# Kernel tuning notes

Hardware: AMD Instinct MI355X
Metric: run time of the kernel (lower is better)

Reference implementation:

```python
import jax, jax.numpy as jnp
import numpy as np

L = 2        # num_layers
D = 512      # d_model
H = 8        # heads
C = 512      # GAT per-head out channels (= d_model, concat=False -> mean over heads)
B, S, E = 4, 512, 4096
NEG = jnp.float32(-1e9)


def setup_inputs() -> dict:
    key = jax.random.key(0)
    ks = jax.random.split(key, 20)
    sc = 0.02  # weight init scale
    inp = {
        'x': jax.random.normal(ks[0], (B, S, D), jnp.float32),
        'Wq': jax.random.normal(ks[1], (L, D, D), jnp.float32) * sc,
        'bq': jnp.zeros((L, D), jnp.float32),
        'Wk': jax.random.normal(ks[2], (L, D, D), jnp.float32) * sc,
        'bk': jnp.zeros((L, D), jnp.float32),
        'Wv': jax.random.normal(ks[3], (L, D, D), jnp.float32) * sc,
        'bv': jnp.zeros((L, D), jnp.float32),
        'Wo': jax.random.normal(ks[4], (L, D, D), jnp.float32) * sc,
        'bo': jnp.zeros((L, D), jnp.float32),
        'gatW': jax.random.normal(ks[5], (L, D, H * C), jnp.float32) * sc,
        'att_src': jax.random.normal(ks[6], (L, H, C), jnp.float32) * sc,
        'att_dst': jax.random.normal(ks[7], (L, H, C), jnp.float32) * sc,
        'gat_bias': jnp.zeros((L, C), jnp.float32),
        'ln_g': jnp.ones((L, D), jnp.float32),
        'ln_b': jnp.zeros((L, D), jnp.float32),
        'input_len': jax.random.randint(ks[8], (B,), S // 2, S + 1, jnp.int32),
        'edges': jax.random.randint(ks[9], (B, 2, E), 0, S // 2, jnp.int32),
        'edge_num': jax.random.randint(ks[10], (B,), E // 2, E + 1, jnp.int32),
    }
    return inp


def layer_norm(x, g, b, eps=1e-5):
    m = x.mean(-1, keepdims=True)
    v = ((x - m) ** 2).mean(-1, keepdims=True)
    return (x - m) * jax.lax.rsqrt(v + eps) * g + b


def mha(x, pad_mask, Wq, bq, Wk, bk, Wv, bv, Wo, bo):
    # pad_mask: [B,S] True where padded (masked out)
    b, s, d = x.shape
    dh = d // H
    q = (x @ Wq + bq).reshape(b, s, H, dh)
    k = (x @ Wk + bk).reshape(b, s, H, dh)
    v = (x @ Wv + bv).reshape(b, s, H, dh)
    scores = jnp.einsum('bqhd,bkhd->bhqk', q, k) / jnp.float32(np.sqrt(dh))
    scores = jnp.where(pad_mask[:, None, None, :], NEG, scores)
    a = jax.nn.softmax(scores, axis=-1)
    o = jnp.einsum('bhqk,bkhd->bqhd', a, v).reshape(b, s, d)
    return o @ Wo + bo


def gat_single(x, edge_index, edge_mask, node_mask, W, a_src_w, a_dst_w, bias):
    # x: [S,D]; edge_index: [2,E]; GATConv(d_model,d_model,heads,concat=False)
    s = x.shape[0]
    h = (x @ W).reshape(s, H, C)
    a_src_n = (h * a_src_w).sum(-1)  # [S,H]
    a_dst_n = (h * a_dst_w).sum(-1)  # [S,H]
    # add self loops (PyG default) for valid nodes
    ar = jnp.arange(s, dtype=edge_index.dtype)
    src = jnp.concatenate([edge_index[0], ar])
    dst = jnp.concatenate([edge_index[1], ar])
    em = jnp.concatenate([edge_mask, node_mask])  # [E+S]
    alpha = jax.nn.leaky_relu(a_src_n[src] + a_dst_n[dst], 0.2)  # [E+S,H]
    alpha = jnp.where(em[:, None], alpha, NEG)
    amax = jax.ops.segment_max(alpha, dst, num_segments=s)  # [S,H]
    ex = jnp.exp(alpha - amax[dst]) * em[:, None].astype(alpha.dtype)
    denom = jax.ops.segment_sum(ex, dst, num_segments=s)
    coef = ex / (denom[dst] + 1e-16)
    msg = h[src] * coef[:, :, None]  # [E+S,H,C]
    out = jax.ops.segment_sum(msg, dst, num_segments=s)  # [S,H,C]
    return out.mean(axis=1) + bias  # concat=False -> mean over heads


def reference(x, Wq, bq, Wk, bk, Wv, bv, Wo, bo, gatW, att_src, att_dst,
              gat_bias, ln_g, ln_b, input_len, edges, edge_num):
    b, s, d = x.shape
    node_mask = jnp.arange(s)[None, :] < input_len[:, None]      # [B,S]
    edge_mask = jnp.arange(edges.shape[-1])[None, :] < edge_num[:, None]  # [B,E]
    pad_mask = ~node_mask
    out = x
    layer_outputs = []
    gat_b = jax.vmap(gat_single, in_axes=(0, 0, 0, 0, None, None, None, None))
    for i in range(L):
        out = mha(out, pad_mask, Wq[i], bq[i], Wk[i], bk[i], Wv[i], bv[i], Wo[i], bo[i])
        g = gat_b(out, edges, edge_mask, node_mask,
                  gatW[i], att_src[i], att_dst[i], gat_bias[i])
        y = jax.nn.relu(layer_norm(g, ln_g[i], ln_b[i])) + out
        out = jnp.where(node_mask[:, :, None], y, out)
        layer_outputs.append(out)
    return jnp.stack(layer_outputs)  # [L,B,S,D]
```

## Files before the change

### kernel.cpp

```cpp
#include <hip/hip_runtime.h>
#include <cstddef>

#define DMODEL 512
#define HEADS  8
#define DH     64
#define CCH    512
#define BATCH  4
#define SEQ    512
#define NEDGE  4096
#define NLAYER 2
#define HC     (HEADS*CCH)

typedef unsigned short bf16_t;
typedef __attribute__((ext_vector_type(8))) short short8;
typedef __attribute__((ext_vector_type(4))) float floatx4;

__device__ __forceinline__ bf16_t f2bf(float f){
  unsigned u = __float_as_uint(f);
  unsigned r = (u + 0x7FFFu + ((u>>16)&1u)) >> 16;
  return (bf16_t)r;
}
__device__ __forceinline__ float bf2f(bf16_t u){ return __uint_as_float(((unsigned)u)<<16); }

__global__ void k_zero(int* __restrict__ p, int n){
  int i = blockIdx.x*256 + threadIdx.x;
  if (i < n) p[i] = 0;
}

__global__ void k_f2b(const float* __restrict__ in, bf16_t* __restrict__ out, int n4){
  int i = blockIdx.x*256 + threadIdx.x;
  if (i < n4){
    float4 v = ((const float4*)in)[i];
    ushort4 o;
    o.x=f2bf(v.x); o.y=f2bf(v.y); o.z=f2bf(v.z); o.w=f2bf(v.w);
    ((ushort4*)out)[i]=o;
  }
}

__global__ __launch_bounds__(256) void k_wt(const float* __restrict__ W, bf16_t* __restrict__ WT,
                                            int K, int N){
  __shared__ float T[32][65];
  int n0 = blockIdx.x*64, k0 = blockIdx.y*32;
  int tid = threadIdx.x;
  int lk = tid>>3, ln = (tid&7)*8;
  const float* src = W + (size_t)(k0+lk)*N + n0 + ln;
  float4 v0 = *(const float4*)src;
  float4 v1 = *(const float4*)(src+4);
  T[lk][ln+0]=v0.x; T[lk][ln+1]=v0.y; T[lk][ln+2]=v0.z; T[lk][ln+3]=v0.w;
  T[lk][ln+4]=v1.x; T[lk][ln+5]=v1.y; T[lk][ln+6]=v1.z; T[lk][ln+7]=v1.w;
  __syncthreads();
  int wn = tid>>2, wk = (tid&3)*8;
  ushort4 o0, o1;
  o0.x=f2bf(T[wk+0][wn]); o0.y=f2bf(T[wk+1][wn]); o0.z=f2bf(T[wk+2][wn]); o0.w=f2bf(T[wk+3][wn]);
  o1.x=f2bf(T[wk+4][wn]); o1.y=f2bf(T[wk+5][wn]); o1.z=f2bf(T[wk+6][wn]); o1.w=f2bf(T[wk+7][wn]);
  bf16_t* dst = WT + (size_t)(n0+wn)*K + k0 + wk;
  *(ushort4*)dst = o0;
  *(ushort4*)(dst+4) = o1;
}

struct GemmB {
  const bf16_t* W; const float* bias; float* C; bf16_t* Cb;
  const float* att_s; const float* att_d; float* asrc; float* adst;
};
struct GemmB3 { GemmB g[3]; };

template<int BM, int BN>
__global__ __launch_bounds__(256) void k_gemm_mfma(const bf16_t* __restrict__ A, GemmB3 p,
                                                   int N, int K){
  constexpr int MI = BM/32;
  constexpr int NJ = BN/32;
  constexpr int ACH = BM/64;
  constexpr int BCH = BN/64;
  const GemmB& g = p.g[blockIdx.z];
  const bf16_t* Wt  = g.W;
  const float* bias = g.bias;
  float* C          = g.C;
  bf16_t* Cb        = g.Cb;
  __shared__ __align__(16) bf16_t As[BM*40];
  __shared__ __align__(16) bf16_t Bs[BN*40];
  int bm = blockIdx.x*BM, bn = blockIdx.y*BN;
  int tid = threadIdx.x;
  int wave = tid>>6, lane = tid&63;
  int wy = wave>>1, wx = wave&1;
  int quad = lane>>4, l16 = lane&15;
  floatx4 acc[MI][NJ];
  #pragma unroll
  for (int i=0;i<MI;i++)
    #pragma unroll
    for (int j=0;j<NJ;j++) acc[i][j] = (floatx4){0.f,0.f,0.f,0.f};
  int sr = tid>>2;
  int sc = (tid&3)<<3;
  for (int k0=0;k0<K;k0+=32){
    uint4 av[ACH], bv[BCH];
    #pragma unroll
    for (int c=0;c<ACH;c++) av[c] = *(const uint4*)(A  + (size_t)(bm+sr+c*64)*K + k0 + sc);
    #pragma unroll
    for (int c=0;c<BCH;c++) bv[c] = *(const uint4*)(Wt + (size_t)(bn+sr+c*64)*K + k0 + sc);
    __syncthreads();
    #pragma unroll
    for (int c=0;c<ACH;c++) *(uint4*)(As + (size_t)(sr+c*64)*40 + sc) = av[c];
    #pragma unroll
    for (int c=0;c<BCH;c++) *(uint4*)(Bs + (size_t)(sr+c*64)*40 + sc) = bv[c];
    __syncthreads();
    short8 af[MI], bfr[NJ];
    #pragma unroll
    for (int i=0;i<MI;i++) af[i]  = *(const short8*)(As + (size_t)(wy*(BM/2)+i*16+l16)*40 + quad*8);
    #pragma unroll
    for (int j=0;j<NJ;j++) bfr[j] = *(const short8*)(Bs + (size_t)(wx*(BN/2)+j*16+l16)*40 + quad*8);
    #pragma unroll
    for (int i=0;i<MI;i++)
      #pragma unroll
      for (int j=0;j<NJ;j++)
        acc[i][j] = __builtin_amdgcn_mfma_f32_16x16x32_bf16(af[i], bfr[j], acc[i][j], 0,0,0);
  }
  #pragma unroll
  for (int i=0;i<MI;i++){
    int row = bm + wy*(BM/2) + i*16 + quad*4;
    #pragma unroll
    for (int j=0;j<NJ;j++){
      int col = bn + wx*(BN/2) + j*16 + l16;
      float bi = bias ? bias[col] : 0.f;
      #pragma unroll
      for (int r=0;r<4;r++){
        float vvv = acc[i][j][r] + bi;
        if (C)  C[(size_t)(row+r)*N + col] = vvv;
        if (Cb) Cb[(size_t)(row+r)*N + col] = f2bf(vvv);
      }
    }
  }
  if (g.asrc){
    int colbase = bn + wx*(BN/2);
    int hidx = colbase >> 9;
    float aw_s[NJ], aw_d[NJ];
    #pragma unroll
    for (int j=0;j<NJ;j++){
      int col = colbase + j*16 + l16;
      aw_s[j] = g.att_s[col];
      aw_d[j] = g.att_d[col];
    }
    #pragma unroll
    for (int i=0;i<MI;i++){
      #pragma unroll
      for (int r=0;r<4;r++){
        float ps=0.f, pd=0.f;
        #pragma unroll
        for (int j=0;j<NJ;j++){ ps += acc[i][j][r]*aw_s[j]; pd += acc[i][j][r]*aw_d[j]; }
        #pragma unroll
        for (int m2=1;m2<16;m2<<=1){ ps += __shfl_xor(ps,m2); pd += __shfl_xor(pd,m2); }
        if (l16==0){
          int row = bm + wy*(BM/2) + i*16 + quad*4 + r;
          atomicAdd(&g.asrc[row*HEADS + hidx], ps);
          atomicAdd(&g.adst[row*HEADS + hidx], pd);
        }
      }
    }
  }
}

__global__ __launch_bounds__(256) void k_attn_flash(const bf16_t* __restrict__ q,
    const bf16_t* __restrict__ k, const bf16_t* __restrict__ v,
    const int* __restrict__ input_len, bf16_t* __restrict__ o){
  __shared__ __align__(16) bf16_t Kt[64*72];
  __shared__ __align__(16) bf16_t Vt[64*72];
  __shared__ __align__(16) bf16_t Pt[4][16*72];
  int q0 = blockIdx.x*64;
  int h  = blockIdx.y, b = blockIdx.z;
  int len = input_len[b];
  int tid = threadIdx.x;
  int w = tid>>6, lane = tid&63;
  int quad = lane>>4, l16 = lane&15;
  const bf16_t* qrow = q + ((size_t)(b*SEQ + q0 + w*16 + l16))*DMODEL + h*DH;
  short8 qa0 = *(const short8*)(qrow + quad*8);
  short8 qa1 = *(const short8*)(qrow + quad*8 + 32);
  int kr = tid>>2, kc = (tid&3)<<4;
  int vr = lane,   vc = w<<4;
  const bf16_t* kbase = k + ((size_t)(b*SEQ))*DMODEL + h*DH;
  const bf16_t* vbase = v + ((size_t)(b*SEQ))*DMODEL + h*DH;
  floatx4 oacc[4];
  #pragma unroll
  for (int dt=0;dt<4;dt++) oacc[dt] = (floatx4){0.f,0.f,0.f,0.f};
  float mrun[4], lrun[4];
  #pragma unroll
  for (int r=0;r<4;r++){ mrun[r]=-1e30f; lrun[r]=0.f; }
  for (int kt=0; kt<SEQ; kt+=64){
    if (kt >= len) break;
    uint4 kv0 = *(const uint4*)(kbase + (size_t)(kt+kr)*DMODEL + kc);
    uint4 kv1 = *(const uint4*)(kbase + (size_t)(kt+kr)*DMODEL + kc + 8);
    uint4 vv0 = *(const uint4*)(vbase + (size_t)(kt+vr)*DMODEL + vc);
    uint4 vv1 = *(const uint4*)(vbase + (size_t)(kt+vr)*DMODEL + vc + 8);
    __syncthreads();
    *(uint4*)(Kt + kr*72 + kc)     = kv0;
    *(uint4*)(Kt + kr*72 + kc + 8) = kv1;
    const ushort* vp0 = (const ushort*)&vv0;
    const ushort* vp1 = (const ushort*)&vv1;
    #pragma unroll
    for (int i2=0;i2<8;i2++) Vt[(vc+i2)*72 + vr]   = vp0[i2];
    #pragma unroll
    for (int i2=0;i2<8;i2++) Vt[(vc+8+i2)*72 + vr] = vp1[i2];
    __syncthreads();
    floatx4 sacc[4];
    #pragma unroll
    for (int nt=0;nt<4;nt++){
      sacc[nt] = (floatx4){0.f,0.f,0.f,0.f};
      short8 kb0 = *(const short8*)(Kt + (nt*16+l16)*72 + quad*8);
      short8 kb1 = *(const short8*)(Kt + (nt*16+l16)*72 + quad*8 + 32);
      sacc[nt] = __builtin_amdgcn_mfma_f32_16x16x32_bf16(qa0, kb0, sacc[nt], 0,0,0);
      sacc[nt] = __builtin_amdgcn_mfma_f32_16x16x32_bf16(qa1, kb1, sacc[nt], 0,0,0);
    }
    #pragma unroll
    for (int nt=0;nt<4;nt++){
      bool valid = (kt + nt*16 + l16) < len;
      #pragma unroll
      for (int r=0;r<4;r++){
        float sv = sacc[nt][r]*0.125f;
        sacc[nt][r] = valid ? sv : -1e30f;
      }
    }
    float alpha[4];
    #pragma unroll
    for (int r=0;r<4;r++){
      float mx = fmaxf(fmaxf(sacc[0][r],sacc[1][r]), fmaxf(sacc[2][r],sacc[3][r]));
      #pragma unroll
      for (int off=1; off<16; off<<=1) mx = fmaxf(mx, __shfl_xor(mx, off));
      float mn = fmaxf(mrun[r], mx);
      alpha[r] = __expf(mrun[r]-mn);
      mrun[r] = mn;
      float rs = 0.f;
      #pragma unroll
      for (int nt=0;nt<4;nt++){
        float pp = __expf(sacc[nt][r]-mn);
        sacc[nt][r] = pp; rs += pp;
      }
      #pragma unroll
      for (int off=1; off<16; off<<=1) rs += __shfl_xor(rs, off);
      lrun[r] = lrun[r]*alpha[r] + rs;
    }
    #pragma unroll
    for (int dt=0;dt<4;dt++)
      #pragma unroll
      for (int r=0;r<4;r++) oacc[dt][r] *= alpha[r];
    bf16_t* pw = Pt[w];
    #pragma unroll
    for (int nt=0;nt<4;nt++)
      #pragma unroll
      for (int r=0;r<4;r++) pw[(quad*4+r)*72 + nt*16 + l16] = f2bf(sacc[nt][r]);
    short8 pa0 = *(const short8*)(pw + l16*72 + quad*8);
    short8 pa1 = *(const short8*)(pw + l16*72 + quad*8 + 32);
    #pragma unroll
    for (int dt=0;dt<4;dt++){
      short8 vb0 = *(const short8*)(Vt + (dt*16+l16)*72 + quad*8);
      short8 vb1 = *(const short8*)(Vt + (dt*16+l16)*72 + quad*8 + 32);
      oacc[dt] = __builtin_amdgcn_mfma_f32_16x16x32_bf16(pa0, vb0, oacc[dt], 0,0,0);
      oacc[dt] = __builtin_amdgcn_mfma_f32_16x16x32_bf16(pa1, vb1, oacc[dt], 0,0,0);
    }
  }
  bf16_t* obase = o + ((size_t)(b*SEQ + q0 + w*16 + quad*4))*DMODEL + h*DH;
  #pragma unroll
  for (int r=0;r<4;r++){
    float invl = 1.f/lrun[r];
    #pragma unroll
    for (int dt=0;dt<4;dt++)
      obase[(size_t)r*DMODEL + dt*16 + l16] = f2bf(oacc[dt][r]*invl);
  }
}

__global__ void k_count(const int* __restrict__ edges, const int* __restrict__ edge_num, int* __restrict__ cnt){
  int b = blockIdx.y;
  int e = blockIdx.x*256 + threadIdx.x;
  if (e >= NEDGE || e >= edge_num[b]) return;
  int dst = edges[(size_t)b*2*NEDGE + NEDGE + e];
  atomicAdd(&cnt[b*SEQ + dst], 1);
}
__global__ void k_prefix(const int* __restrict__ cnt, int* __restrict__ offs, int* __restrict__ cursor){
  if (threadIdx.x==0){
    int b = blockIdx.x, acc=0;
    for (int s=0;s<SEQ;s++){ offs[b*SEQ+s]=acc; cursor[b*SEQ+s]=acc; acc+=cnt[b*SEQ+s]; }
  }
}
__global__ void k_fill(const int* __restrict__ edges, const int* __restrict__ edge_num,
                       int* __restrict__ cursor, int* __restrict__ elist){
  int b = blockIdx.y;
  int e = blockIdx.x*256 + threadIdx.x;
  if (e >= NEDGE || e >= edge_num[b]) return;
  int dst = edges[(size_t)b*2*NEDGE + NEDGE + e];
  int pos = atomicAdd(&cursor[b*SEQ + dst], 1);
  elist[(size_t)b*NEDGE + pos] = e;
}

__global__ __launch_bounds__(256) void k_gat_agg(const bf16_t* __restrict__ hbuf,
    const float* __restrict__ asrc, const float* __restrict__ adst,
    const int* __restrict__ offs, const int* __restrict__ cnt, const int* __restrict__ elist,
    const int* __restrict__ edges, const int* __restrict__ input_len,
    const float* __restrict__ gat_bias, float* __restrict__ gout){
  int s = blockIdx.x, b = blockIdx.y;
  if (s >= input_len[b]) return;
  __shared__ float amax_s[8], den_s[8], adl[8];
  __shared__ float cf[32][8];
  __shared__ int   cs[32];
  int tid = threadIdx.x;
  int n = cnt[b*SEQ+s];
  const int* el = elist + (size_t)b*NEDGE + offs[b*SEQ+s];
  const int* srcrow = edges + (size_t)b*2*NEDGE;
  if (tid < 8) adl[tid] = adst[(b*SEQ+s)*HEADS + tid];
  __syncthreads();
  if (tid < 64){
    float mx[8];
    #pragma unroll
    for (int h2=0;h2<8;h2++) mx[h2] = -1e30f;
    for (int j = tid; j <= n; j += 64){
      int src = (j==n) ? s : srcrow[el[j]];
      const float* ap = asrc + (size_t)(b*SEQ+src)*HEADS;
      #pragma unroll
      for (int h2=0;h2<8;h2++){
        float a = ap[h2] + adl[h2];
        a = (a>0.f)? a : 0.2f*a;
        mx[h2] = fmaxf(mx[h2], a);
      }
    }
    #pragma unroll
    for (int h2=0;h2<8;h2++){
      float vmx = mx[h2];
      #pragma unroll
      for (int off=32; off; off>>=1) vmx = fmaxf(vmx, __shfl_xor(vmx,off,64));
      mx[h2]=vmx;
    }
    float sm[8];
    #pragma unroll
    for (int h2=0;h2<8;h2++) sm[h2]=0.f;
    for (int j = tid; j <= n; j += 64){
      int src = (j==n) ? s : srcrow[el[j]];
      const float* ap = asrc + (size_t)(b*SEQ+src)*HEADS;
      #pragma unroll
      for (int h2=0;h2<8;h2++){
        float a = ap[h2] + adl[h2];
        a = (a>0.f)? a : 0.2f*a;
        sm[h2] += __expf(a - mx[h2]);
      }
    }
    #pragma unroll
    for (int h2=0;h2<8;h2++){
      float vs = sm[h2];
      #pragma unroll
      for (int off=32; off; off>>=1) vs += __shfl_xor(vs,off,64);
      if (tid==0){ amax_s[h2]=mx[h2]; den_s[h2]=vs; }
    }
  }
  __syncthreads();
  float acc0=0.f, acc1=0.f;
  int c0 = tid*2;
  for (int j0=0; j0 <= n; j0 += 32){
    int jm = min(32, n+1-j0);
    if (tid < jm*8){
      int jj = j0 + (tid>>3), h2 = tid&7;
      int src = (jj==n) ? s : srcrow[el[jj]];
      if (h2==0) cs[tid>>3] = src;
      float a = asrc[(size_t)(b*SEQ+src)*HEADS + h2] + adl[h2];
      a = (a>0.f)? a : 0.2f*a;
      cf[tid>>3][h2] = __expf(a - amax_s[h2]) / (den_s[h2] + 1e-16f);
    }
    __syncthreads();
    for (int jj=0; jj<jm; ++jj){
      int src = cs[jj];
      const bf16_t* hrow = hbuf + ((size_t)(b*SEQ+src))*HC;
      #pragma unroll
      for (int h2=0;h2<8;h2++){
        float wgt = cf[jj][h2];
        ushort2 hv = *(const ushort2*)(hrow + h2*CCH + c0);
        acc0 += wgt * bf2f(hv.x);
        acc1 += wgt * bf2f(hv.y);
      }
    }
    __syncthreads();
  }
  size_t gbse = ((size_t)(b*SEQ+s))*CCH;
  float2 outv = { acc0*0.125f + gat_bias[c0], acc1*0.125f + gat_bias[c0+1] };
  *(float2*)(gout + gbse + c0) = outv;
}

__global__ __launch_bounds__(256) void k_combine(const float* __restrict__ gbuf, const float* __restrict__ xin,
    const float* __restrict__ lng, const float* __restrict__ lnb,
    const int* __restrict__ input_len, bf16_t* __restrict__ curb, float* __restrict__ outp){
  __shared__ float red[256];
  int s = blockIdx.x, b = blockIdx.y, tid = threadIdx.x;
  size_t row = ((size_t)(b*SEQ+s))*DMODEL;
  float x0 = xin[row+tid], x1 = xin[row+tid+256];
  float y0 = x0, y1 = x1;
  if (s < input_len[b]){
    float g0 = gbuf[row+tid], g1 = gbuf[row+tid+256];
    red[tid] = g0+g1;
    __syncthreads();
    for (int off=128; off; off>>=1){ if (tid<off) red[tid]+=red[tid+off]; __syncthreads(); }
    float mean = red[0]*(1.f/512.f);
    __syncthreads();
    float d0 = g0-mean, d1 = g1-mean;
    red[tid] = d0*d0 + d1*d1;
    __syncthreads();
    for (int off=128; off; off>>=1){ if (tid<off) red[tid]+=red[tid+off]; __syncthreads(); }
    float inv = rsqrtf(red[0]*(1.f/512.f) + 1e-5f);
    float t0 = d0*inv*lng[tid]     + lnb[tid];
    float t1 = d1*inv*lng[tid+256] + lnb[tid+256];
    y0 = fmaxf(t0,0.f) + x0;
    y1 = fmaxf(t1,0.f) + x1;
  }
  curb[row+tid]=f2bf(y0); curb[row+tid+256]=f2bf(y1);
  outp[row+tid]=y0; outp[row+tid+256]=y1;
}

extern "C" void kernel_launch(void* const* d_in, const int* in_sizes, int n_in,
                              void* d_out, int out_size, void* d_ws, size_t ws_size,
                              hipStream_t stream){
  (void)in_sizes; (void)n_in; (void)out_size; (void)ws_size;
  const float* x       = (const float*)d_in[0];
  const float* Wq      = (const float*)d_in[1];
  const float* bq      = (const float*)d_in[2];
  const float* Wk      = (const float*)d_in[3];
  const float* bk      = (const float*)d_in[4];
  const float* Wv      = (const float*)d_in[5];
  const float* bv      = (const float*)d_in[6];
  const float* Wo      = (const float*)d_in[7];
  const float* bo      = (const float*)d_in[8];
  const float* gatW    = (const float*)d_in[9];
  const float* att_src = (const float*)d_in[10];
  const float* att_dst = (const float*)d_in[11];
  const float* gat_bias= (const float*)d_in[12];
  const float* ln_g    = (const float*)d_in[13];
  const float* ln_b    = (const float*)d_in[14];
  const int* input_len  = (const int*)d_in[15];
  const int* edges      = (const int*)d_in[16];
  const int* edge_num   = (const int*)d_in[17];
  float* outp = (float*)d_out;

  char* w = (char*)d_ws;
  size_t off = 0;
  auto alloc = [&](size_t bytes)->char*{ char* p = w + off; off += (bytes + 255) & ~(size_t)255; return p; };
  const size_t BSD = (size_t)BATCH*SEQ*DMODEL;
  const size_t BSH = (size_t)BATCH*SEQ*HEADS;
  float* mha  = (float*)alloc(BSD*4);
  bf16_t* hb  = (bf16_t*)alloc((size_t)BATCH*SEQ*HC*2);
  float* gb   = (float*)alloc(BSD*4);
  float* attn_nodes = (float*)alloc(2*BSH*4);
  float* asrc = attn_nodes;
  float* adst = attn_nodes + BSH;
  int* cnt    = (int*)alloc(BATCH*SEQ*4);
  int* offs   = (int*)alloc(BATCH*SEQ*4);
  int* cursor = (int*)alloc(BATCH*SEQ*4);
  int* elist  = (int*)alloc((size_t)BATCH*NEDGE*4);
  bf16_t* xbf  = (bf16_t*)alloc(BSD*2);
  bf16_t* curb = (bf16_t*)alloc(BSD*2);
  bf16_t* qbf  = (bf16_t*)alloc(BSD*2);
  bf16_t* kbf  = (bf16_t*)alloc(BSD*2);
  bf16_t* vbf  = (bf16_t*)alloc(BSD*2);
  bf16_t* obf  = (bf16_t*)alloc(BSD*2);
  bf16_t* abf  = (bf16_t*)alloc(BSD*2);
  bf16_t* wqt  = (bf16_t*)alloc((size_t)NLAYER*DMODEL*DMODEL*2);
  bf16_t* wkt  = (bf16_t*)alloc((size_t)NLAYER*DMODEL*DMODEL*2);
  bf16_t* wvt  = (bf16_t*)alloc((size_t)NLAYER*DMODEL*DMODEL*2);
  bf16_t* wot  = (bf16_t*)alloc((size_t)NLAYER*DMODEL*DMODEL*2);
  bf16_t* gwt  = (bf16_t*)alloc((size_t)NLAYER*DMODEL*HC*2);

  k_zero<<<dim3((BATCH*SEQ+255)/256),256,0,stream>>>(cnt, BATCH*SEQ);
  k_count<<<dim3(NEDGE/256, BATCH),256,0,stream>>>(edges, edge_num, cnt);
  k_prefix<<<dim3(BATCH),64,0,stream>>>(cnt, offs, cursor);
  k_fill<<<dim3(NEDGE/256, BATCH),256,0,stream>>>(edges, edge_num, cursor, elist);

  for (int i=0;i<NLAYER;i++){
    size_t wo = (size_t)i*DMODEL*DMODEL;
    dim3 gsq(DMODEL/64, DMODEL/32);
    k_wt<<<gsq,256,0,stream>>>(Wq+wo, wqt+wo, DMODEL, DMODEL);
    k_wt<<<gsq,256,0,stream>>>(Wk+wo, wkt+wo, DMODEL, DMODEL);
    k_wt<<<gsq,256,0,stream>>>(Wv+wo, wvt+wo, DMODEL, DMODEL);
    k_wt<<<gsq,256,0,stream>>>(Wo+wo, wot+wo, DMODEL, DMODEL);
    size_t go = (size_t)i*DMODEL*HC;
    k_wt<<<dim3(HC/64, DMODEL/32),256,0,stream>>>(gatW+go, gwt+go, DMODEL, HC);
  }
  k_f2b<<<dim3((unsigned)(BSD/4/256)),256,0,stream>>>(x, xbf, (int)(BSD/4));

  const int M = BATCH*SEQ;
  for (int i=0;i<NLAYER;i++){
    size_t wo = (size_t)i*DMODEL*DMODEL;
    size_t bo2 = (size_t)i*DMODEL;
    const bf16_t* Ab = (i==0) ? xbf : curb;
    GemmB3 qkv;
    qkv.g[0] = { wqt+wo, bq+bo2, nullptr, qbf, nullptr, nullptr, nullptr, nullptr };
    qkv.g[1] = { wkt+wo, bk+bo2, nullptr, kbf, nullptr, nullptr, nullptr, nullptr };
    qkv.g[2] = { wvt+wo, bv+bo2, nullptr, vbf, nullptr, nullptr, nullptr, nullptr };
    k_gemm_mfma<64,64><<<dim3(M/64, DMODEL/64, 3),256,0,stream>>>(Ab, qkv, DMODEL, DMODEL);
    k_attn_flash<<<dim3(SEQ/64, HEADS, BATCH),256,0,stream>>>(qbf, kbf, vbf, input_len, obf);
    GemmB3 og;
    og.g[0] = { wot+wo, bo+bo2, mha, abf, nullptr, nullptr, nullptr, nullptr };
    og.g[1] = og.g[0]; og.g[2] = og.g[0];
    k_gemm_mfma<64,64><<<dim3(M/64, DMODEL/64, 1),256,0,stream>>>(obf, og, DMODEL, DMODEL);
    k_zero<<<dim3((unsigned)((2*BSH+255)/256)),256,0,stream>>>((int*)attn_nodes, (int)(2*BSH));
    GemmB3 gg;
    gg.g[0] = { gwt + (size_t)i*DMODEL*HC, nullptr, nullptr, hb,
                att_src + (size_t)i*HC, att_dst + (size_t)i*HC, asrc, adst };
    gg.g[1] = gg.g[0]; gg.g[2] = gg.g[0];
    k_gemm_mfma<64,64><<<dim3(M/64, HC/64, 1),256,0,stream>>>(abf, gg, HC, DMODEL);
    k_gat_agg<<<dim3(SEQ, BATCH),256,0,stream>>>(hb, asrc, adst, offs, cnt, elist, edges, input_len, gat_bias + (size_t)i*CCH, gb);
    k_combine<<<dim3(SEQ, BATCH),256,0,stream>>>(gb, mha, ln_g+bo2, ln_b+bo2, input_len, curb, outp + (size_t)i*BSD);
  }
}
```

Measured before the change: 351.4 us.

## Double-buffer GEMM shared tiles and batch all weight transposes into one launch

The MFMA GEMM now uses two shared-memory buffers per operand and prefetches the next K-slice from global memory into registers while the current slice is being multiplied. This cuts one barrier per iteration and hides global load latency behind the MFMAs. Separately, the ten per-weight transpose/convert launches are merged into a single grid that picks the weight matrix from the block index, which removes launch overhead. The cost is twice the GEMM shared-memory footprint, which may lower occupancy.

Result: faster. 331.1 us (-5.8%).

```diff
diff --git a/kernel.cpp b/kernel.cpp
--- a/kernel.cpp
+++ b/kernel.cpp
@@ -37,10 +37,16 @@
   }
 }
 
-__global__ __launch_bounds__(256) void k_wt(const float* __restrict__ W, bf16_t* __restrict__ WT,
-                                            int K, int N){
+struct WtJob { const float* W[10]; bf16_t* WT[10]; };
+__global__ __launch_bounds__(256) void k_wt_all(WtJob j){
   __shared__ float T[32][65];
-  int n0 = blockIdx.x*64, k0 = blockIdx.y*32;
+  int t = blockIdx.x, k0 = blockIdx.y*32;
+  int wsel, n0, N;
+  if (t < 64){ wsel = t>>3; n0 = (t&7)*64; N = 512; }
+  else { int t2 = t-64; wsel = 8 + (t2>>6); n0 = (t2&63)*64; N = 4096; }
+  const float* W = j.W[wsel];
+  bf16_t* WT = j.WT[wsel];
+  const int K = 512;
   int tid = threadIdx.x;
   int lk = tid>>3, ln = (tid&7)*8;
   const float* src = W + (size_t)(k0+lk)*N + n0 + ln;
@@ -76,8 +82,8 @@
   const float* bias = g.bias;
   float* C          = g.C;
   bf16_t* Cb        = g.Cb;
-  __shared__ __align__(16) bf16_t As[BM*40];
-  __shared__ __align__(16) bf16_t Bs[BN*40];
+  __shared__ __align__(16) bf16_t As[2][BM*40];
+  __shared__ __align__(16) bf16_t Bs[2][BN*40];
   int bm = blockIdx.x*BM, bn = blockIdx.y*BN;
   int tid = threadIdx.x;
   int wave = tid>>6, lane = tid&63;
@@ -90,28 +96,47 @@
     for (int j=0;j<NJ;j++) acc[i][j] = (floatx4){0.f,0.f,0.f,0.f};
   int sr = tid>>2;
   int sc = (tid&3)<<3;
-  for (int k0=0;k0<K;k0+=32){
-    uint4 av[ACH], bv[BCH];
-    #pragma unroll
-    for (int c=0;c<ACH;c++) av[c] = *(const uint4*)(A  + (size_t)(bm+sr+c*64)*K + k0 + sc);
-    #pragma unroll
-    for (int c=0;c<BCH;c++) bv[c] = *(const uint4*)(Wt + (size_t)(bn+sr+c*64)*K + k0 + sc);
-    __syncthreads();
-    #pragma unroll
-    for (int c=0;c<ACH;c++) *(uint4*)(As + (size_t)(sr+c*64)*40 + sc) = av[c];
-    #pragma unroll
-    for (int c=0;c<BCH;c++) *(uint4*)(Bs + (size_t)(sr+c*64)*40 + sc) = bv[c];
-    __syncthreads();
+  const bf16_t* Aptr = A  + (size_t)(bm+sr)*K + sc;
+  const bf16_t* Bptr = Wt + (size_t)(bn+sr)*K + sc;
+  uint4 av[ACH], bv[BCH];
+  #pragma unroll
+  for (int c=0;c<ACH;c++) av[c] = *(const uint4*)(Aptr + (size_t)c*64*K);
+  #pragma unroll
+  for (int c=0;c<BCH;c++) bv[c] = *(const uint4*)(Bptr + (size_t)c*64*K);
+  #pragma unroll
+  for (int c=0;c<ACH;c++) *(uint4*)(As[0] + (size_t)(sr+c*64)*40 + sc) = av[c];
+  #pragma unroll
+  for (int c=0;c<BCH;c++) *(uint4*)(Bs[0] + (size_t)(sr+c*64)*40 + sc) = bv[c];
+  int nk = K>>5;
+  for (int kk=0; kk<nk; kk++){
+    __syncthreads();
+    if (kk+1 < nk){
+      int ko = (kk+1)<<5;
+      #pragma unroll
+      for (int c=0;c<ACH;c++) av[c] = *(const uint4*)(Aptr + (size_t)c*64*K + ko);
+      #pragma unroll
+      for (int c=0;c<BCH;c++) bv[c] = *(const uint4*)(Bptr + (size_t)c*64*K + ko);
+    }
+    const bf16_t* Ab = As[kk&1];
+    const bf16_t* Bb = Bs[kk&1];
     short8 af[MI], bfr[NJ];
     #pragma unroll
-    for (int i=0;i<MI;i++) af[i]  = *(const short8*)(As + (size_t)(wy*(BM/2)+i*16+l16)*40 + quad*8);
-    #pragma unroll
-    for (int j=0;j<NJ;j++) bfr[j] = *(const short8*)(Bs + (size_t)(wx*(BN/2)+j*16+l16)*40 + quad*8);
+    for (int i=0;i<MI;i++) af[i]  = *(const short8*)(Ab + (size_t)(wy*(BM/2)+i*16+l16)*40 + quad*8);
+    #pragma unroll
+    for (int j=0;j<NJ;j++) bfr[j] = *(const short8*)(Bb + (size_t)(wx*(BN/2)+j*16+l16)*40 + quad*8);
     #pragma unroll
     for (int i=0;i<MI;i++)
       #pragma unroll
       for (int j=0;j<NJ;j++)
         acc[i][j] = __builtin_amdgcn_mfma_f32_16x16x32_bf16(af[i], bfr[j], acc[i][j], 0,0,0);
+    if (kk+1 < nk){
+      bf16_t* Aw = As[(kk+1)&1];
+      bf16_t* Bw = Bs[(kk+1)&1];
+      #pragma unroll
+      for (int c=0;c<ACH;c++) *(uint4*)(Aw + (size_t)(sr+c*64)*40 + sc) = av[c];
+      #pragma unroll
+      for (int c=0;c<BCH;c++) *(uint4*)(Bw + (size_t)(sr+c*64)*40 + sc) = bv[c];
+    }
   }
   #pragma unroll
   for (int i=0;i<MI;i++){
@@ -463,16 +488,17 @@
   k_prefix<<<dim3(BATCH),64,0,stream>>>(cnt, offs, cursor);
   k_fill<<<dim3(NEDGE/256, BATCH),256,0,stream>>>(edges, edge_num, cursor, elist);
 
+  WtJob wj;
   for (int i=0;i<NLAYER;i++){
     size_t wo = (size_t)i*DMODEL*DMODEL;
-    dim3 gsq(DMODEL/64, DMODEL/32);
-    k_wt<<<gsq,256,0,stream>>>(Wq+wo, wqt+wo, DMODEL, DMODEL);
-    k_wt<<<gsq,256,0,stream>>>(Wk+wo, wkt+wo, DMODEL, DMODEL);
-    k_wt<<<gsq,256,0,stream>>>(Wv+wo, wvt+wo, DMODEL, DMODEL);
-    k_wt<<<gsq,256,0,stream>>>(Wo+wo, wot+wo, DMODEL, DMODEL);
+    wj.W[i*4+0]=Wq+wo;  wj.WT[i*4+0]=wqt+wo;
+    wj.W[i*4+1]=Wk+wo;  wj.WT[i*4+1]=wkt+wo;
+    wj.W[i*4+2]=Wv+wo;  wj.WT[i*4+2]=wvt+wo;
+    wj.W[i*4+3]=Wo+wo;  wj.WT[i*4+3]=wot+wo;
     size_t go = (size_t)i*DMODEL*HC;
-    k_wt<<<dim3(HC/64, DMODEL/32),256,0,stream>>>(gatW+go, gwt+go, DMODEL, HC);
-  }
+    wj.W[8+i]=gatW+go;  wj.WT[8+i]=gwt+go;
+  }
+  k_wt_all<<<dim3(192, 16),256,0,stream>>>(wj);
   k_f2b<<<dim3((unsigned)(BSD/4/256)),256,0,stream>>>(x, xbf, (int)(BSD/4));
 
   const int M = BATCH*SEQ;
```
